# Kernel tuning notes

Hardware: AMD Instinct MI355X
Metric: run time of the kernel (lower is better)

## Reference

```python
import jax, jax.numpy as jnp
import numpy as np

B, N, IN_DIM, OUT_DIM, H = 8, 1024, 256, 256, 8
D = OUT_DIM // H  # head_dim = 32
NEG_INF = -1.0e9


def setup_inputs() -> dict:
    key = jax.random.key(0)
    k_x, k_adj, k_W, k_a = jax.random.split(key, 4)
    x = jax.random.normal(k_x, (B, N, IN_DIM), dtype=jnp.float32)
    adj = jax.random.randint(k_adj, (B, N, N), 0, 2, dtype=jnp.int32)
    # nn.Linear(in_dim, out_dim, bias=False): weight [out_dim, in_dim]
    lim = 1.0 / np.sqrt(IN_DIM)
    W = jax.random.uniform(k_W, (OUT_DIM, IN_DIM), jnp.float32, -lim, lim)
    # a: (1, H, 2*D), xavier_uniform with gain=1.414
    gain = 1.414
    bound = gain * np.sqrt(6.0 / (H + 2 * D))
    a = jax.random.uniform(k_a, (1, H, 2 * D), jnp.float32, -bound, bound)
    return {"x": x, "adj": adj, "W": W, "a": a}


def reference(x, adj, W, a):
    Bn, Nn, _ = x.shape
    h = jnp.einsum('bni,oi->bno', x, W).reshape(Bn, Nn, H, D)  # [B,N,H,D]
    # sum(cat(h_i, h_j) * a) = h_i . a_src + h_j . a_dst  (avoids O(N^2*2D) concat)
    a_src = a[0, :, :D]   # [H,D] multiplies h_i (query/row index i)
    a_dst = a[0, :, D:]   # [H,D] multiplies h_j (key/col index j)
    s_i = jnp.einsum('bnhd,hd->bnh', h, a_src)  # [B,N,H]
    s_j = jnp.einsum('bnhd,hd->bnh', h, a_dst)  # [B,N,H]
    e = s_i[:, :, None, :] + s_j[:, None, :, :]  # [B,i,j,H]
    e = jnp.where(e > 0, e, 0.2 * e)  # LeakyReLU(0.2)
    mask = (adj != 0)[..., None]      # [B,N,N,1] broadcast over heads
    e = jnp.where(mask, e, NEG_INF)
    alpha = jax.nn.softmax(e, axis=2)  # softmax over j (neighbors)
    # dropout p=0.0 -> identity
    h_prime = jnp.einsum('bijh,bjhd->bihd', alpha, h)
    h_prime = h_prime.reshape(Bn, Nn, H * D)
    return jax.nn.elu(h_prime)
```

## Files before the change

### kernel.cpp

```cpp
#include <hip/hip_runtime.h>
#include <cmath>

namespace {
constexpr int B = 8, N = 1024, IND = 256, OUTD = 256, H = 8, D = 32;
constexpr float LOG2E = 1.4426950408889634f;
}

typedef __attribute__((ext_vector_type(8))) short short8v;
typedef __attribute__((ext_vector_type(4))) float f32x4;

__device__ inline ushort f2bf(float f) {
  __bf16 b = (__bf16)f;
  return __builtin_bit_cast(ushort, b);
}
__device__ inline float bf2f(ushort u) {
  return __uint_as_float((uint)u << 16);
}

__global__ __launch_bounds__(256) void gat_pre(const int* __restrict__ adj,
                                               const float* __restrict__ W,
                                               const float* __restrict__ a,
                                               uint* __restrict__ bitsT,
                                               ushort* __restrict__ Wfh,
                                               ushort* __restrict__ Wfl,
                                               float* __restrict__ a_s) {
  const int bid = blockIdx.x;
  const int t = threadIdx.x;
  if (bid < 2048) {
    const int lane = t & 63, w = t >> 6;
    const int wid = bid * 4 + w;
    const int b = wid >> 10, i = wid & 1023;
    const int4* ap = (const int4*)(adj + ((size_t)b * N + i) * N);
#pragma unroll
    for (int c = 0; c < 4; ++c) {
      const int4 v = ap[c * 64 + lane];
      uint val = (v.x != 0 ? 1u : 0u) | (v.y != 0 ? 2u : 0u) |
                 (v.z != 0 ? 4u : 0u) | (v.w != 0 ? 8u : 0u);
      val <<= (lane & 7) * 4;
      val |= (uint)__shfl_xor((int)val, 1);
      val |= (uint)__shfl_xor((int)val, 2);
      val |= (uint)__shfl_xor((int)val, 4);
      if ((lane & 7) == 0) {
        const int jt = c * 8 + (lane >> 3);
        bitsT[((size_t)b * 32 + jt) * N + i] = val;
      }
    }
  } else {
    const int idx = (bid - 2048) * 256 + t;
    const int e = idx & 7, l = (idx >> 3) & 63, ct = (idx >> 9) & 15,
              kb = idx >> 13;
    const int c = ct * 16 + (l & 15);
    const int k = kb * 32 + (l >> 4) * 8 + e;
    const float v = W[c * IND + k];
    const ushort hi = f2bf(v);
    Wfh[idx] = hi;
    Wfl[idx] = f2bf(v - bf2f(hi));
    if (idx < 512) a_s[idx] = a[idx] * LOG2E;
  }
}

__global__ __launch_bounds__(256) void gat_gemm(
    const float* __restrict__ x, const ushort* __restrict__ Wfh,
    const ushort* __restrict__ Wfl, const float* __restrict__ a_s,
    float* __restrict__ siT, float* __restrict__ sjT,
    ushort* __restrict__ hTbF) {
  __shared__ __align__(16) char smem[17664];
  float(*xs)[36] = (float(*)[36])smem;
  ushort* wsh = (ushort*)(smem + 9216);
  ushort* wsl = (ushort*)(smem + 13312);
  float(*tile2)[65] = (float(*)[65])smem;

  const int t = threadIdx.x, lane = t & 63, w = t >> 6;
  const int la = lane & 15, g = lane >> 4;
  const int bid = blockIdx.x;
  const int work = ((bid & 7) << 6) + (bid >> 3);
  const int bx = work >> 2, by = work & 3;

  f32x4 z = {0.f, 0.f, 0.f, 0.f};
  f32x4 acc[4] = {z, z, z, z};

  const float* xp = x + (size_t)(bx * 64 + (t >> 2)) * IND + (t & 3) * 8;
  const ushort* wgh = Wfh + (size_t)(by * 4) * 512;
  const ushort* wgl = Wfl + (size_t)(by * 4) * 512;

  for (int kb = 0; kb < 8; ++kb) {
    __syncthreads();
    {
      float4 v0 = *(const float4*)(xp + kb * 32);
      float4 v1 = *(const float4*)(xp + kb * 32 + 4);
      float* dst = &xs[t >> 2][(t & 3) * 8];
      *(float4*)dst = v0;
      *(float4*)(dst + 4) = v1;
    }
    *(short8v*)&wsh[t * 8] = *(const short8v*)(wgh + (size_t)kb * 8192 + t * 8);
    *(short8v*)&wsl[t * 8] = *(const short8v*)(wgl + (size_t)kb * 8192 + t * 8);
    __syncthreads();

    const float* xr = &xs[w * 16 + la][g * 8];
    float4 u0 = *(const float4*)(xr);
    float4 u1 = *(const float4*)(xr + 4);
    const float af[8] = {u0.x, u0.y, u0.z, u0.w, u1.x, u1.y, u1.z, u1.w};
    short8v ah, al;
#pragma unroll
    for (int e = 0; e < 8; ++e) {
      const ushort hb = f2bf(af[e]);
      ah[e] = (short)hb;
      al[e] = (short)f2bf(af[e] - bf2f(hb));
    }
#pragma unroll
    for (int ct = 0; ct < 4; ++ct) {
      const short8v bh = *(const short8v*)&wsh[ct * 512 + lane * 8];
      const short8v bl = *(const short8v*)&wsl[ct * 512 + lane * 8];
      acc[ct] = __builtin_amdgcn_mfma_f32_16x16x32_bf16(ah, bh, acc[ct], 0, 0, 0);
      acc[ct] = __builtin_amdgcn_mfma_f32_16x16x32_bf16(al, bh, acc[ct], 0, 0, 0);
      acc[ct] = __builtin_amdgcn_mfma_f32_16x16x32_bf16(ah, bl, acc[ct], 0, 0, 0);
    }
  }

  const int batch = bx >> 4;
  const int nbase = (bx & 15) * 64 + w * 16;

#pragma unroll
  for (int hp2 = 0; hp2 < 2; ++hp2) {
    const int head = by * 2 + hp2;
    const float a0 = a_s[head * 64 + la];
    const float a1 = a_s[head * 64 + 16 + la];
    const float a2 = a_s[head * 64 + 32 + la];
    const float a3 = a_s[head * 64 + 48 + la];
    float s1v[4], s2v[4];
#pragma unroll
    for (int q = 0; q < 4; ++q) {
      s1v[q] = acc[hp2 * 2][q] * a0 + acc[hp2 * 2 + 1][q] * a1;
      s2v[q] = acc[hp2 * 2][q] * a2 + acc[hp2 * 2 + 1][q] * a3;
    }
#pragma unroll
    for (int mask = 1; mask <= 8; mask <<= 1)
#pragma unroll
      for (int q = 0; q < 4; ++q) {
        s1v[q] += __shfl_xor(s1v[q], mask);
        s2v[q] += __shfl_xor(s2v[q], mask);
      }
    if (la == 0) {
#pragma unroll
      for (int q = 0; q < 4; ++q) {
        const size_t o = (size_t)(batch * H + head) * N + nbase + g * 4 + q;
        siT[o] = s1v[q];
        sjT[o] = s2v[q];
      }
    }
  }

  __syncthreads();
#pragma unroll
  for (int ct = 0; ct < 4; ++ct)
#pragma unroll
    for (int q = 0; q < 4; ++q)
      tile2[w * 16 + g * 4 + q][ct * 16 + la] = acc[ct][q];
  __syncthreads();

  const int jt0 = (bx & 15) * 2;
#pragma unroll
  for (int s = 0; s < 2; ++s) {
    const int gg = t * 2 + s;
    const int head = gg >> 8, rem = gg & 255;
    const int jt_loc = rem >> 7, half = (rem >> 6) & 1, l = rem & 63;
    const int d = half * 16 + (l & 15);
    short8v pk;
#pragma unroll
    for (int e = 0; e < 8; ++e)
      pk[e] = (short)f2bf(tile2[jt_loc * 32 + (l >> 4) * 8 + e][head * 32 + d]);
    const int bh_g = batch * H + by * 2 + head;
    *(short8v*)(hTbF + ((size_t)(bh_g * 32 + jt0 + jt_loc) * 64 + l) * 16 + half * 8) = pk;
  }
}

__global__ __launch_bounds__(256) void gat_agg(
    const uint* __restrict__ bitsT, const float* __restrict__ siT,
    const float* __restrict__ sjT, const ushort* __restrict__ hTbF,
    float* __restrict__ out) {
  __shared__ float part[2][64][13];
  const int t = threadIdx.x;
  const int lane = t & 63, w = t >> 6;
  const int iw = w & 1, jq = w >> 1;
  const int bid = blockIdx.x;
  const int work = ((bid & 7) << 8) + (bid >> 3);
  const int bh = work >> 5;
  const int itg = work & 31;
  const int b = bh >> 3, hh = bh & 7;
  const int i0 = itg * 32 + iw * 16;
  const int la = lane & 15, g = lane >> 4;
  const int iA = i0 + la;

  const float si_r = siT[(size_t)bh * N + iA];
  const uint* btp = bitsT + (size_t)b * 32 * N + (size_t)jq * 16 * N + iA;
  const float* sjp = sjT + (size_t)bh * N + jq * 512 + g * 8;
  const ushort* hp = hTbF + (size_t)bh * 32768 + (size_t)jq * 16384 + lane * 16;

  f32x4 acc0 = {0.f, 0.f, 0.f, 0.f}, acc1 = {0.f, 0.f, 0.f, 0.f};
  f32x4 accl = {0.f, 0.f, 0.f, 0.f};
  short8v ones;
#pragma unroll
  for (int e = 0; e < 8; ++e) ones[e] = (short)0x3F80;

  uint bits0, bits1;
  float4 sjA0, sjB0, sjA1, sjB1;
  short8v b00, b10, b01, b11;

#define AGG_LOAD(S, JT)                                      \
  bits##S = btp[(size_t)(JT)*1024];                          \
  sjA##S = *(const float4*)(sjp + (JT) * 32);                \
  sjB##S = *(const float4*)(sjp + (JT) * 32 + 4);            \
  b0##S = *(const short8v*)(hp + (size_t)(JT)*1024);         \
  b1##S = *(const short8v*)(hp + (size_t)(JT)*1024 + 8);

#define AGG_COMP(S)                                                           \
  {                                                                           \
    const uint byte_ = (bits##S >> (g * 8)) & 0xffu;                          \
    const float sjv[8] = {sjA##S.x, sjA##S.y, sjA##S.z, sjA##S.w,             \
                          sjB##S.x, sjB##S.y, sjB##S.z, sjB##S.w};            \
    short8v af;                                                               \
    _Pragma("unroll") for (int e = 0; e < 8; ++e) {                           \
      float s = si_r + sjv[e];                                                \
      s = fmaxf(s, 0.2f * s);                                                 \
      s = ((byte_ >> e) & 1u) ? s : -INFINITY;                                \
      af[e] = (short)f2bf(__builtin_amdgcn_exp2f(s));                         \
    }                                                                         \
    __builtin_amdgcn_s_setprio(1);                                            \
    acc0 = __builtin_amdgcn_mfma_f32_16x16x32_bf16(af, b0##S, acc0, 0, 0, 0); \
    acc1 = __builtin_amdgcn_mfma_f32_16x16x32_bf16(af, b1##S, acc1, 0, 0, 0); \
    accl = __builtin_amdgcn_mfma_f32_16x16x32_bf16(af, ones, accl, 0, 0, 0);  \
    __builtin_amdgcn_s_setprio(0);                                            \
  }

  AGG_LOAD(0, 0)
  AGG_LOAD(1, 1)
#pragma unroll
  for (int jt = 0; jt < 16; jt += 2) {
    AGG_COMP(0)
    if (jt + 2 < 16) { AGG_LOAD(0, jt + 2) }
    AGG_COMP(1)
    if (jt + 3 < 16) { AGG_LOAD(1, jt + 3) }
  }
#undef AGG_LOAD
#undef AGG_COMP

  if (jq == 1) {
    float* p = part[iw][lane];
#pragma unroll
    for (int k = 0; k < 4; ++k) {
      p[k] = acc0[k];
      p[4 + k] = acc1[k];
      p[8 + k] = accl[k];
    }
  }
  __syncthreads();
  if (jq == 0) {
    const float* p = part[iw][lane];
#pragma unroll
    for (int k = 0; k < 4; ++k) {
      acc0[k] += p[k];
      acc1[k] += p[4 + k];
      accl[k] += p[8 + k];
    }
    float* op = out + ((size_t)(b * N + i0)) * OUTD + hh * D;
#pragma unroll
    for (int r = 0; r < 4; ++r) {
      const int ic = g * 4 + r;
      const float li = accl[r];
      float v0 = acc0[r] / li;
      v0 = v0 > 0.f ? v0 : expm1f(v0);
      op[(size_t)ic * OUTD + la] = v0;
      float v1 = acc1[r] / li;
      v1 = v1 > 0.f ? v1 : expm1f(v1);
      op[(size_t)ic * OUTD + 16 + la] = v1;
    }
  }
}

extern "C" void kernel_launch(void* const* d_in, const int* in_sizes, int n_in,
                              void* d_out, int out_size, void* d_ws, size_t ws_size,
                              hipStream_t stream) {
  const float* x = (const float*)d_in[0];
  const int* adj = (const int*)d_in[1];
  const float* W = (const float*)d_in[2];
  const float* a = (const float*)d_in[3];
  float* out = (float*)d_out;

  float* ws = (float*)d_ws;
  float* siT = ws;
  float* sjT = siT + (size_t)B * N * H;
  uint* bitsT = (uint*)(sjT + (size_t)B * N * H);
  ushort* hTbF = (ushort*)(bitsT + (size_t)B * 32 * N);
  ushort* Wfh = hTbF + (size_t)B * N * OUTD;
  ushort* Wfl = Wfh + 131072;
  float* a_s = (float*)(Wfl + 131072);

  gat_pre<<<2048 + 512, 256, 0, stream>>>(adj, W, a, bitsT, Wfh, Wfl, a_s);
  gat_gemm<<<512, 256, 0, stream>>>(x, Wfh, Wfl, a_s, siT, sjT, hTbF);
  gat_agg<<<2048, 256, 0, stream>>>(bitsT, siT, sjT, hTbF, out);
}
```

Baseline: 46.71 us.

## Fuse adjacency bit-packing and projection GEMM into one kernel, splitting W in-loop

Merges the preprocessing kernel and the GEMM kernel into a single launch: the first 512 blocks run the projection GEMM and the remaining 2048 blocks pack the adjacency mask into bits. The GEMM now reads W as fp32 and splits it into bf16 hi/lo parts inside its k-loop, and scales the attention vector by log2(e) inline. This removes one kernel launch, the dependency between the two kernels, and the round trip of the pre-split W through global memory. In exchange, each GEMM block repeats the W conversion work, and the bit-packing blocks now contend for the GPU with the GEMM blocks.

```diff
diff --git a/kernel.cpp b/kernel.cpp
--- a/kernel.cpp
+++ b/kernel.cpp
@@ -17,18 +17,17 @@
   return __uint_as_float((uint)u << 16);
 }
 
-__global__ __launch_bounds__(256) void gat_pre(const int* __restrict__ adj,
-                                               const float* __restrict__ W,
-                                               const float* __restrict__ a,
-                                               uint* __restrict__ bitsT,
-                                               ushort* __restrict__ Wfh,
-                                               ushort* __restrict__ Wfl,
-                                               float* __restrict__ a_s) {
+__global__ __launch_bounds__(256) void gat_k1(
+    const float* __restrict__ x, const float* __restrict__ W,
+    const float* __restrict__ a, const int* __restrict__ adj,
+    uint* __restrict__ bitsT, float* __restrict__ siT,
+    float* __restrict__ sjT, ushort* __restrict__ hTbF) {
   const int bid = blockIdx.x;
   const int t = threadIdx.x;
-  if (bid < 2048) {
+
+  if (bid >= 512) {
     const int lane = t & 63, w = t >> 6;
-    const int wid = bid * 4 + w;
+    const int wid = (bid - 512) * 4 + w;
     const int b = wid >> 10, i = wid & 1023;
     const int4* ap = (const int4*)(adj + ((size_t)b * N + i) * N);
 #pragma unroll
@@ -45,34 +44,17 @@
         bitsT[((size_t)b * 32 + jt) * N + i] = val;
       }
     }
-  } else {
-    const int idx = (bid - 2048) * 256 + t;
-    const int e = idx & 7, l = (idx >> 3) & 63, ct = (idx >> 9) & 15,
-              kb = idx >> 13;
-    const int c = ct * 16 + (l & 15);
-    const int k = kb * 32 + (l >> 4) * 8 + e;
-    const float v = W[c * IND + k];
-    const ushort hi = f2bf(v);
-    Wfh[idx] = hi;
-    Wfl[idx] = f2bf(v - bf2f(hi));
-    if (idx < 512) a_s[idx] = a[idx] * LOG2E;
-  }
-}
-
-__global__ __launch_bounds__(256) void gat_gemm(
-    const float* __restrict__ x, const ushort* __restrict__ Wfh,
-    const ushort* __restrict__ Wfl, const float* __restrict__ a_s,
-    float* __restrict__ siT, float* __restrict__ sjT,
-    ushort* __restrict__ hTbF) {
+    return;
+  }
+
   __shared__ __align__(16) char smem[17664];
   float(*xs)[36] = (float(*)[36])smem;
   ushort* wsh = (ushort*)(smem + 9216);
   ushort* wsl = (ushort*)(smem + 13312);
   float(*tile2)[65] = (float(*)[65])smem;
 
-  const int t = threadIdx.x, lane = t & 63, w = t >> 6;
+  const int lane = t & 63, w = t >> 6;
   const int la = lane & 15, g = lane >> 4;
-  const int bid = blockIdx.x;
   const int work = ((bid & 7) << 6) + (bid >> 3);
   const int bx = work >> 2, by = work & 3;
 
@@ -80,8 +62,9 @@
   f32x4 acc[4] = {z, z, z, z};
 
   const float* xp = x + (size_t)(bx * 64 + (t >> 2)) * IND + (t & 3) * 8;
-  const ushort* wgh = Wfh + (size_t)(by * 4) * 512;
-  const ushort* wgl = Wfl + (size_t)(by * 4) * 512;
+  const int w_c = by * 64 + (t >> 6) * 16 + (t & 15);
+  const int w_k0 = ((t >> 4) & 3) * 8;
+  const float* wp = W + (size_t)w_c * IND + w_k0;
 
   for (int kb = 0; kb < 8; ++kb) {
     __syncthreads();
@@ -92,8 +75,20 @@
       *(float4*)dst = v0;
       *(float4*)(dst + 4) = v1;
     }
-    *(short8v*)&wsh[t * 8] = *(const short8v*)(wgh + (size_t)kb * 8192 + t * 8);
-    *(short8v*)&wsl[t * 8] = *(const short8v*)(wgl + (size_t)kb * 8192 + t * 8);
+    {
+      float4 v0 = *(const float4*)(wp + kb * 32);
+      float4 v1 = *(const float4*)(wp + kb * 32 + 4);
+      const float wf[8] = {v0.x, v0.y, v0.z, v0.w, v1.x, v1.y, v1.z, v1.w};
+      short8v ph, pl;
+#pragma unroll
+      for (int e = 0; e < 8; ++e) {
+        const ushort hi = f2bf(wf[e]);
+        ph[e] = (short)hi;
+        pl[e] = (short)f2bf(wf[e] - bf2f(hi));
+      }
+      *(short8v*)&wsh[t * 8] = ph;
+      *(short8v*)&wsl[t * 8] = pl;
+    }
     __syncthreads();
 
     const float* xr = &xs[w * 16 + la][g * 8];
@@ -123,10 +118,10 @@
 #pragma unroll
   for (int hp2 = 0; hp2 < 2; ++hp2) {
     const int head = by * 2 + hp2;
-    const float a0 = a_s[head * 64 + la];
-    const float a1 = a_s[head * 64 + 16 + la];
-    const float a2 = a_s[head * 64 + 32 + la];
-    const float a3 = a_s[head * 64 + 48 + la];
+    const float a0 = a[head * 64 + la] * LOG2E;
+    const float a1 = a[head * 64 + 16 + la] * LOG2E;
+    const float a2 = a[head * 64 + 32 + la] * LOG2E;
+    const float a3 = a[head * 64 + 48 + la] * LOG2E;
     float s1v[4], s2v[4];
 #pragma unroll
     for (int q = 0; q < 4; ++q) {
@@ -291,11 +286,7 @@
   float* sjT = siT + (size_t)B * N * H;
   uint* bitsT = (uint*)(sjT + (size_t)B * N * H);
   ushort* hTbF = (ushort*)(bitsT + (size_t)B * 32 * N);
-  ushort* Wfh = hTbF + (size_t)B * N * OUTD;
-  ushort* Wfl = Wfh + 131072;
-  float* a_s = (float*)(Wfl + 131072);
-
-  gat_pre<<<2048 + 512, 256, 0, stream>>>(adj, W, a, bitsT, Wfh, Wfl, a_s);
-  gat_gemm<<<512, 256, 0, stream>>>(x, Wfh, Wfl, a_s, siT, sjT, hTbF);
+
+  gat_k1<<<512 + 2048, 256, 0, stream>>>(x, W, a, adj, bitsT, siT, sjT, hTbF);
   gat_agg<<<2048, 256, 0, stream>>>(bitsT, siT, sjT, hTbF, out);
 }
```

After: 42.11 us. 1.11x faster.
